# Kernel optimization log

Measured on AMD Instinct MI355X. Metric: run time of the kernel, lower is better.

The kernel has to match this reference:

```python
import jax, jax.numpy as jnp
import numpy as np

B, T, F, U, L, C = 1024, 100, 300, 512, 2, 10
EPS = 1e-3  # keras LayerNormalization default epsilon


def _ln(z, g, b):
    m = jnp.mean(z, axis=-1, keepdims=True)
    v = jnp.var(z, axis=-1, keepdims=True)
    return (z - m) * jax.lax.rsqrt(v + EPS) * g + b


def _cell(xt, h, c, W, R, bias, kg, kb, rg, rb, sg, sb):
    # LayerNormLSTMCell: LN(x@W) + LN(h@R) + b, gates i,f,g,o; LN on new cell state
    z = _ln(xt @ W, kg, kb) + _ln(h @ R, rg, rb) + bias
    i, f, g, o = jnp.split(z, 4, axis=-1)
    c_new = jax.nn.sigmoid(f) * c + jax.nn.sigmoid(i) * jnp.tanh(g)
    c_new = _ln(c_new, sg, sb)
    h_new = jax.nn.sigmoid(o) * jnp.tanh(c_new)
    return h_new, c_new


def setup_inputs() -> dict:
    key = jax.random.key(0)
    ks = jax.random.split(key, 8 + 2 * L)
    d = {}
    d["x"] = jax.random.normal(ks[0], (B, T, F), jnp.float32)
    lens = jax.random.randint(ks[1], (B,), 1, T + 1)
    d["mask"] = (jnp.arange(T)[None, :] < lens[:, None]).astype(jnp.int32)
    in_dims = [F, U]
    ki = 2
    for l in range(L):
        s = 1.0 / np.sqrt(in_dims[l])
        d[f"W{l}"] = jax.random.uniform(ks[ki], (in_dims[l], 4 * U), jnp.float32, -s, s); ki += 1
        d[f"R{l}"] = jax.random.uniform(ks[ki], (U, 4 * U), jnp.float32, -0.044, 0.044); ki += 1
        d[f"b{l}"] = jnp.zeros((4 * U,), jnp.float32)
        d[f"kg{l}"] = jnp.ones((4 * U,), jnp.float32)
        d[f"kb{l}"] = jnp.zeros((4 * U,), jnp.float32)
        d[f"rg{l}"] = jnp.ones((4 * U,), jnp.float32)
        d[f"rb{l}"] = jnp.zeros((4 * U,), jnp.float32)
        d[f"sg{l}"] = jnp.ones((U,), jnp.float32)
        d[f"sb{l}"] = jnp.zeros((U,), jnp.float32)
    s = 1.0 / np.sqrt(U)
    d["Wd"] = jax.random.uniform(ks[ki], (U, C), jnp.float32, -s, s)
    d["bd"] = jnp.zeros((C,), jnp.float32)
    return d


def _forward(x, mask,
             W0, R0, b0, kg0, kb0, rg0, rb0, sg0, sb0,
             W1, R1, b1, kg1, kb1, rg1, rb1, sg1, sb1,
             Wd, bd):
    params = [
        (W0, R0, b0, kg0, kb0, rg0, rb0, sg0, sb0),
        (W1, R1, b1, kg1, kb1, rg1, rb1, sg1, sb1),
    ]
    bsz = x.shape[0]
    dt = x.dtype

    def step(carry, inp_t):
        states, out_prev = carry
        xt, mt = inp_t  # xt: [B,F], mt: [B] bool
        mb = mt[:, None]
        inp = xt
        new_states = []
        for (h, c), p in zip(states, params):
            hn, cn = _cell(inp, h, c, *p)
            inp = hn
            # Keras RNN masking: carry previous state at masked steps
            new_states.append((jnp.where(mb, hn, h), jnp.where(mb, cn, c)))
        out = jnp.where(mb, inp, out_prev)
        return (tuple(new_states), out), None

    init_states = tuple((jnp.zeros((bsz, U), dt), jnp.zeros((bsz, U), dt)) for _ in range(L))
    carry0 = (init_states, jnp.zeros((bsz, U), dt))
    xs = (jnp.transpose(x, (1, 0, 2)), mask.T.astype(bool))  # time-major
    (_, out), _ = jax.lax.scan(step, carry0, xs)
    return jax.nn.softmax(out @ Wd + bd, axis=-1)


def reference(x, mask,
              W0, R0, b0, kg0, kb0, rg0, rb0, sg0, sb0,
              W1, R1, b1, kg1, kb1, rg1, rb1, sg1, sb1,
              Wd, bd):
    return _forward(x, mask,
                    W0, R0, b0, kg0, kb0, rg0, rb0, sg0, sb0,
                    W1, R1, b1, kg1, kb1, rg1, rb1, sg1, sb1,
                    Wd, bd)
```

## Files before the change

### kernel.cpp

```cpp
#include <hip/hip_runtime.h>

#define B_ 1024
#define T_ 100
#define F_ 300
#define FP_ 320
#define U_ 512
#define G4_ 2048
#define C_ 10
#define EPS_ 1e-3f

typedef _Float16 f16x8 __attribute__((ext_vector_type(8)));
typedef float f32x4 __attribute__((ext_vector_type(4)));

typedef __attribute__((address_space(1))) const void* gcptr_t;
typedef __attribute__((address_space(3))) void* lptr_t;

__device__ __forceinline__ void async_ld16(_Float16* lds, const _Float16* g) {
  __builtin_amdgcn_global_load_lds((gcptr_t)g, (lptr_t)lds, 16, 0, 0);
}

__global__ __launch_bounds__(1024) void prep_kernel(const int* __restrict__ mask,
                                                    int* __restrict__ perm,
                                                    int* __restrict__ nt) {
  __shared__ int cnt[T_ + 1];
  __shared__ int start[T_ + 1];
  int b = threadIdx.x;
  if (b <= T_) cnt[b] = 0;
  __syncthreads();
  const int* mrow = mask + (size_t)b * T_;
  int len = 0;
  for (int t = 0; t < T_; t++) len += mrow[t];
  atomicAdd(&cnt[len], 1);
  __syncthreads();
  if (b == 0) {
    int run = 0;
    for (int l = T_; l >= 0; l--) {
      start[l] = run;
      run += cnt[l];
    }
  }
  __syncthreads();
  if (b < T_) nt[b] = start[b];
  __syncthreads();
  int pos = atomicAdd(&start[len], 1);
  perm[pos] = b;
}


__global__ __launch_bounds__(256) void cast_x_kernel(const float* __restrict__ x,
                                                     const int* __restrict__ perm,
                                                     const int* __restrict__ nt,
                                                     _Float16* __restrict__ xhi,
                                                     _Float16* __restrict__ xlo) {
  size_t cidx = (size_t)blockIdx.x * 256 + threadIdx.x;
  int fc = (int)(cidx % (FP_ / 8));
  size_t bt = cidx / (FP_ / 8);
  int i = (int)(bt % B_);
  int t = (int)(bt / B_);
  int nr = (nt[t] + 127) & ~127;
  if (i >= nr) return;
  int b = perm[i];
  int f = fc * 8;
  const float* xr = x + ((size_t)b * T_ + t) * F_;
  float v[8];
  if (f + 8 <= F_) {
    float4 a = *(const float4*)(xr + f);
    float4 c = *(const float4*)(xr + f + 4);
    v[0] = a.x; v[1] = a.y; v[2] = a.z; v[3] = a.w;
    v[4] = c.x; v[5] = c.y; v[6] = c.z; v[7] = c.w;
  } else {
#pragma unroll
    for (int j = 0; j < 8; j++) v[j] = (f + j < F_) ? xr[f + j] : 0.f;
  }
  f16x8 hi, lo;
#pragma unroll
  for (int j = 0; j < 8; j++) {
    _Float16 h = (_Float16)v[j];
    hi[j] = h;
    lo[j] = (_Float16)(v[j] - (float)h);
  }
  *(f16x8*)(xhi + cidx * 8) = hi;
  *(f16x8*)(xlo + cidx * 8) = lo;
}

__global__ __launch_bounds__(256) void cast_w_kernel(const float* __restrict__ W,
                                                     _Float16* __restrict__ Whi,
                                                     _Float16* __restrict__ Wlo,
                                                     int K, int N, int Kp) {
  __shared__ float tile[32][33];
  int n0 = blockIdx.x * 32, k0 = blockIdx.y * 32;
  int tx = threadIdx.x & 31, ty = threadIdx.x >> 5;
#pragma unroll
  for (int r = 0; r < 32; r += 8) {
    int k = k0 + ty + r;
    tile[ty + r][tx] = (k < K) ? W[(size_t)k * N + n0 + tx] : 0.f;
  }
  __syncthreads();
#pragma unroll
  for (int r = 0; r < 32; r += 8) {
    int n = n0 + ty + r, kk = k0 + tx;
    if (kk < Kp) {
      float v = tile[tx][ty + r];
      _Float16 h = (_Float16)v;
      Whi[(size_t)n * Kp + kk] = h;
      Wlo[(size_t)n * Kp + kk] = (_Float16)(v - (float)h);
    }
  }
}

struct GemmOp {
  const _Float16* A;
  const _Float16* Bt;
  float* G;
  int lda;
  int K;
  size_t aLo;
  int step;
};
struct G4Pack {
  GemmOp op[4];
  const int* nt;
};

__global__ __launch_bounds__(256) void gemm_phase(G4Pack P) {
  GemmOp op = P.op[blockIdx.z];
  const int mBase = blockIdx.y * 128, nBase = blockIdx.x * 128;
  if (mBase >= P.nt[op.step]) return;
  const int K = op.K, lda = op.lda;
  const _Float16* A = op.A;
  const _Float16* Bt = op.Bt;

  __shared__ __align__(16) _Float16 as[128][64];
  __shared__ __align__(16) _Float16 bs[128][64];

  const int tid = threadIdx.x;
  const int w = tid >> 6;
  const int lane = tid & 63;
  const int wm = (w & 1) << 6;
  const int wn = (w >> 1) << 6;

  f32x4 acc[4][4];
#pragma unroll
  for (int mt = 0; mt < 4; mt++)
#pragma unroll
    for (int nt2 = 0; nt2 < 4; nt2++) acc[mt][nt2] = (f32x4){0.f, 0.f, 0.f, 0.f};

  const size_t bLo = (size_t)G4_ * K;
#pragma unroll 1
  for (int s = 0; s < 3; s++) {
    const _Float16* Ap = A + ((s == 1) ? op.aLo : 0);
    const _Float16* Bp = Bt + ((s == 2) ? bLo : 0);
#pragma unroll 1
    for (int k0 = 0; k0 < K; k0 += 64) {
#pragma unroll
      for (int j = 0; j < 4; j++) {
        int i = (w << 2) + j;
        int idx = (i << 6) + lane;
        int row = idx >> 3;
        int cl = ((idx & 7) ^ (row & 7)) << 3;
        async_ld16(&as[0][0] + (i << 9),
                   Ap + (size_t)(mBase + row) * lda + k0 + cl);
      }
#pragma unroll
      for (int j = 0; j < 4; j++) {
        int i = (w << 2) + j;
        int idx = (i << 6) + lane;
        int row = idx >> 3;
        int cl = ((idx & 7) ^ (row & 7)) << 3;
        async_ld16(&bs[0][0] + (i << 9),
                   Bp + (size_t)(nBase + row) * K + k0 + cl);
      }
      __syncthreads();
#pragma unroll
      for (int q = 0; q < 2; q++) {
        f16x8 af[4], bf[4];
#pragma unroll
        for (int mt = 0; mt < 4; mt++) {
          int row = wm + (mt << 4) + (lane & 15);
          int p = ((q << 2) + (lane >> 4)) ^ (row & 7);
          af[mt] = *(const f16x8*)&as[row][p << 3];
        }
#pragma unroll
        for (int nt2 = 0; nt2 < 4; nt2++) {
          int row = wn + (nt2 << 4) + (lane & 15);
          int p = ((q << 2) + (lane >> 4)) ^ (row & 7);
          bf[nt2] = *(const f16x8*)&bs[row][p << 3];
        }
#pragma unroll
        for (int mt = 0; mt < 4; mt++)
#pragma unroll
          for (int nt2 = 0; nt2 < 4; nt2++)
            acc[mt][nt2] = __builtin_amdgcn_mfma_f32_16x16x32_f16(af[mt], bf[nt2], acc[mt][nt2], 0, 0, 0);
      }
      __syncthreads();
    }
  }
  int q4 = lane >> 4, c = lane & 15;
  float* G = op.G;
#pragma unroll
  for (int mt = 0; mt < 4; mt++)
#pragma unroll
    for (int nt2 = 0; nt2 < 4; nt2++)
#pragma unroll
      for (int r = 0; r < 4; r++) {
        int row = mBase + wm + (mt << 4) + (q4 << 2) + r;
        int col = nBase + wn + (nt2 << 4) + c;
        G[(size_t)row * G4_ + col] = acc[mt][nt2][r];
      }
}


__device__ __forceinline__ void block_reduce(float* v, int n, float* sred, int tid) {
  int lane = tid & 63, w = tid >> 6;
  for (int off = 32; off > 0; off >>= 1)
    for (int i = 0; i < n; i++) v[i] += __shfl_down(v[i], off, 64);
  if (lane == 0)
    for (int i = 0; i < n; i++) sred[w * 4 + i] = v[i];
  __syncthreads();
  if (tid == 0)
    for (int i = 0; i < n; i++) sred[16 + i] = sred[i] + sred[4 + i] + sred[8 + i] + sred[12 + i];
  __syncthreads();
  for (int i = 0; i < n; i++) v[i] = sred[16 + i];
}

__device__ __forceinline__ float sigm(float x) { return 1.f / (1.f + expf(-x)); }

struct CellOp {
  const float* Gx;
  const float* Gh;
  const float* bias;
  const float* kg;
  const float* kb;
  const float* rg;
  const float* rb;
  const float* sg;
  const float* sb;
  float* cS;
  _Float16* hP;
  _Float16* hnP;
  float* outb;
  int step;
};
struct C2Pack {
  CellOp op[2];
  const int* nt;
};

__global__ __launch_bounds__(256) void cell_phase(C2Pack P) {
  CellOp cp = P.op[blockIdx.x >> 10];
  int b = blockIdx.x & (B_ - 1);
  if (b >= P.nt[cp.step]) return;
  int tid = threadIdx.x;
  __shared__ float sred[20];
  const float* gx = cp.Gx + (size_t)b * G4_;
  const float* gh = cp.Gh + (size_t)b * G4_;
  float vx[8], vh[8];
  float s[4] = {0.f, 0.f, 0.f, 0.f};
#pragma unroll
  for (int i = 0; i < 8; i++) {
    int col = tid + (i << 8);
    float a = gx[col], d = gh[col];
    vx[i] = a;
    vh[i] = d;
    s[0] += a;
    s[1] += a * a;
    s[2] += d;
    s[3] += d * d;
  }
  block_reduce(s, 4, sred, tid);
  const float inv = 1.f / 2048.f;
  float m1 = s[0] * inv, m2 = s[2] * inv;
  float rs1 = rsqrtf(fmaxf(s[1] * inv - m1 * m1, 0.f) + EPS_);
  float rs2 = rsqrtf(fmaxf(s[3] * inv - m2 * m2, 0.f) + EPS_);
  float z[8];
#pragma unroll
  for (int i = 0; i < 8; i++) {
    int col = tid + (i << 8);
    z[i] = (vx[i] - m1) * rs1 * cp.kg[col] + cp.kb[col] +
           (vh[i] - m2) * rs2 * cp.rg[col] + cp.rb[col] + cp.bias[col];
  }
  int j0 = tid, j1 = tid + 256;
  size_t base = (size_t)b * U_;
  _Float16* hHi = cp.hP;
  _Float16* hLo = cp.hP + (size_t)B_ * U_;
  float co0 = cp.cS[base + j0], co1 = cp.cS[base + j1];
  float cn0 = sigm(z[2]) * co0 + sigm(z[0]) * tanhf(z[4]);
  float cn1 = sigm(z[3]) * co1 + sigm(z[1]) * tanhf(z[5]);
  float t2[2] = {cn0 + cn1, cn0 * cn0 + cn1 * cn1};
  block_reduce(t2, 2, sred, tid);
  const float invU = 1.f / 512.f;
  float mc = t2[0] * invU;
  float rsc = rsqrtf(fmaxf(t2[1] * invU - mc * mc, 0.f) + EPS_);
  float cl0 = (cn0 - mc) * rsc * cp.sg[j0] + cp.sb[j0];
  float cl1 = (cn1 - mc) * rsc * cp.sg[j1] + cp.sb[j1];
  float hn0 = sigm(z[6]) * tanhf(cl0);
  float hn1 = sigm(z[7]) * tanhf(cl1);
  _Float16 hh0 = (_Float16)hn0, hh1 = (_Float16)hn1;
  hHi[base + j0] = hh0;
  hLo[base + j0] = (_Float16)(hn0 - (float)hh0);
  hHi[base + j1] = hh1;
  hLo[base + j1] = (_Float16)(hn1 - (float)hh1);
  cp.cS[base + j0] = cl0;
  cp.cS[base + j1] = cl1;
  if (cp.hnP) {
    _Float16* nHi = cp.hnP;
    _Float16* nLo = cp.hnP + (size_t)B_ * U_;
    nHi[base + j0] = hh0;
    nLo[base + j0] = (_Float16)(hn0 - (float)hh0);
    nHi[base + j1] = hh1;
    nLo[base + j1] = (_Float16)(hn1 - (float)hh1);
  }
  if (cp.outb) {
    cp.outb[base + j0] = hn0;
    cp.outb[base + j1] = hn1;
  }
}

__global__ __launch_bounds__(64) void dense_softmax_kernel(const float* __restrict__ outb,
                                                           const float* __restrict__ Wd,
                                                           const float* __restrict__ bd,
                                                           const int* __restrict__ perm,
                                                           float* __restrict__ o) {
  int b = blockIdx.x, lane = threadIdx.x;
  __shared__ float sl[16];
  int col = lane & 15, kg = lane >> 4;
  float acc = 0.f;
  if (col < C_) {
    for (int k = kg; k < U_; k += 4) acc += outb[(size_t)b * U_ + k] * Wd[(size_t)k * C_ + col];
  }
  acc += __shfl_down(acc, 16, 64);
  acc += __shfl_down(acc, 32, 64);
  if (lane < C_) sl[lane] = acc + bd[lane];
  __syncthreads();
  if (lane < C_) {
    float mx = sl[0];
    for (int i = 1; i < C_; i++) mx = fmaxf(mx, sl[i]);
    float ssum = 0.f;
    for (int i = 0; i < C_; i++) ssum += expf(sl[i] - mx);
    o[(size_t)perm[b] * C_ + lane] = expf(sl[lane] - mx) / ssum;
  }
}


extern "C" void kernel_launch(void* const* d_in, const int* in_sizes, int n_in,
                              void* d_out, int out_size, void* d_ws, size_t ws_size,
                              hipStream_t stream) {
  const float* x = (const float*)d_in[0];
  const int* mask = (const int*)d_in[1];
  const float* W0 = (const float*)d_in[2];
  const float* R0 = (const float*)d_in[3];
  const float* b0 = (const float*)d_in[4];
  const float* kg0 = (const float*)d_in[5];
  const float* kb0 = (const float*)d_in[6];
  const float* rg0 = (const float*)d_in[7];
  const float* rb0 = (const float*)d_in[8];
  const float* sg0 = (const float*)d_in[9];
  const float* sb0 = (const float*)d_in[10];
  const float* W1 = (const float*)d_in[11];
  const float* R1 = (const float*)d_in[12];
  const float* b1 = (const float*)d_in[13];
  const float* kg1 = (const float*)d_in[14];
  const float* kb1 = (const float*)d_in[15];
  const float* rg1 = (const float*)d_in[16];
  const float* rb1 = (const float*)d_in[17];
  const float* sg1 = (const float*)d_in[18];
  const float* sb1 = (const float*)d_in[19];
  const float* Wd = (const float*)d_in[20];
  const float* bd = (const float*)d_in[21];
  float* out = (float*)d_out;

  char* w = (char*)d_ws;
  size_t o = 0;
  auto alloc = [&](size_t bytes) {
    size_t r = o;
    o += (bytes + 255) & ~(size_t)255;
    return r;
  };
  size_t o_c0s = alloc((size_t)B_ * U_ * 4);
  size_t o_c1s = alloc((size_t)B_ * U_ * 4);
  size_t o_outf = alloc((size_t)B_ * U_ * 4);
  size_t o_h0p = alloc((size_t)B_ * U_ * 2 * 2);
  size_t o_h1p = alloc((size_t)B_ * U_ * 2 * 2);
  size_t o_G0h = alloc((size_t)B_ * G4_ * 4);
  size_t zero_bytes = o;
  size_t o_hn0p = alloc((size_t)B_ * U_ * 2 * 2);
  size_t o_xh = alloc((size_t)T_ * B_ * FP_ * 2 * 2);
  size_t o_W0t = alloc((size_t)G4_ * FP_ * 2 * 2);
  size_t o_R0t = alloc((size_t)G4_ * U_ * 2 * 2);
  size_t o_W1t = alloc((size_t)G4_ * U_ * 2 * 2);
  size_t o_R1t = alloc((size_t)G4_ * U_ * 2 * 2);
  size_t o_G0x = alloc((size_t)B_ * G4_ * 4);
  size_t o_G1x = alloc((size_t)B_ * G4_ * 4);
  size_t o_G1h = alloc((size_t)B_ * G4_ * 4);
  size_t o_perm = alloc((size_t)B_ * 4);
  size_t o_nt = alloc((size_t)T_ * 4);
  (void)ws_size;

  float* c0s = (float*)(w + o_c0s);
  float* c1s = (float*)(w + o_c1s);
  float* outf = (float*)(w + o_outf);
  _Float16* h0p = (_Float16*)(w + o_h0p);
  _Float16* h1p = (_Float16*)(w + o_h1p);
  float* G0h = (float*)(w + o_G0h);
  _Float16* hn0p = (_Float16*)(w + o_hn0p);
  _Float16* xh = (_Float16*)(w + o_xh);
  _Float16* W0t = (_Float16*)(w + o_W0t);
  _Float16* R0t = (_Float16*)(w + o_R0t);
  _Float16* W1t = (_Float16*)(w + o_W1t);
  _Float16* R1t = (_Float16*)(w + o_R1t);
  float* G0x = (float*)(w + o_G0x);
  float* G1x = (float*)(w + o_G1x);
  float* G1h = (float*)(w + o_G1h);
  int* perm = (int*)(w + o_perm);
  int* ntp = (int*)(w + o_nt);

  hipMemsetAsync(w, 0, zero_bytes, stream);

  prep_kernel<<<1, 1024, 0, stream>>>(mask, perm, ntp);

  {
    size_t chunks = (size_t)T_ * B_ * (FP_ / 8);
    cast_x_kernel<<<dim3((unsigned)(chunks / 256)), 256, 0, stream>>>(
        x, perm, ntp, xh, xh + (size_t)T_ * B_ * FP_);
  }
  cast_w_kernel<<<dim3(G4_ / 32, FP_ / 32), 256, 0, stream>>>(
      W0, W0t, W0t + (size_t)G4_ * FP_, F_, G4_, FP_);
  cast_w_kernel<<<dim3(G4_ / 32, U_ / 32), 256, 0, stream>>>(
      R0, R0t, R0t + (size_t)G4_ * U_, U_, G4_, U_);
  cast_w_kernel<<<dim3(G4_ / 32, U_ / 32), 256, 0, stream>>>(
      W1, W1t, W1t + (size_t)G4_ * U_, U_, G4_, U_);
  cast_w_kernel<<<dim3(G4_ / 32, U_ / 32), 256, 0, stream>>>(
      R1, R1t, R1t + (size_t)G4_ * U_, U_, G4_, U_);

  const size_t xLoOff = (size_t)T_ * B_ * FP_;
  const size_t hLoOff = (size_t)B_ * U_;

  auto xw_op = [&](int t) -> GemmOp {
    return GemmOp{xh + (size_t)t * B_ * FP_, W0t, G0x, FP_, FP_, xLoOff, t};
  };
  CellOp cell0op = {G0x, G0h, b0, kg0, kb0, rg0, rb0, sg0, sb0,
                    c0s, h0p, hn0p, nullptr, 0};
  CellOp cell1op = {G1x, G1h, b1, kg1, kb1, rg1, rb1, sg1, sb1,
                    c1s, h1p, nullptr, outf, 0};

  {
    G4Pack P;
    P.nt = ntp;
    P.op[0] = xw_op(0);
    P.op[1] = P.op[0];
    P.op[2] = P.op[0];
    P.op[3] = P.op[0];
    gemm_phase<<<dim3(G4_ / 128, B_ / 128, 1), 256, 0, stream>>>(P);
    C2Pack CP;
    CP.nt = ntp;
    cell0op.step = 0;
    CP.op[0] = cell0op;
    CP.op[1] = cell0op;
    cell_phase<<<B_, 256, 0, stream>>>(CP);
  }

  for (int t = 0; t < T_; t++) {
    bool more = (t < T_ - 1);
    G4Pack P;
    P.nt = ntp;
    P.op[0] = GemmOp{hn0p, W1t, G1x, U_, U_, hLoOff, t};
    P.op[1] = GemmOp{h1p, R1t, G1h, U_, U_, hLoOff, t};
    if (more) {
      P.op[2] = GemmOp{h0p, R0t, G0h, U_, U_, hLoOff, t + 1};
      P.op[3] = xw_op(t + 1);
    } else {
      P.op[2] = P.op[0];
      P.op[3] = P.op[0];
    }
    gemm_phase<<<dim3(G4_ / 128, B_ / 128, more ? 4 : 2), 256, 0, stream>>>(P);

    C2Pack CP;
    CP.nt = ntp;
    cell1op.step = t;
    CP.op[0] = cell1op;
    cell0op.step = t + 1;
    CP.op[1] = more ? cell0op : cell1op;
    cell_phase<<<more ? 2 * B_ : B_, 256, 0, stream>>>(CP);
  }

  dense_softmax_kernel<<<B_, 64, 0, stream>>>(outf, Wd, bd, perm, out);
}
```

Measured before the change: 4.194 ms.

## Fuse split-fp16 hi/lo GEMM passes into a single K loop

The three sequential passes over K (hi*hi, lo*hi, hi*lo) become one loop. Each iteration loads the hi and lo tiles of both A and B into four LDS buffers and issues three MFMAs per fragment pair. This removes two extra K sweeps of loop overhead, barriers and redundant reloads of the hi tiles. It also raises MFMA priority with s_setprio. The cost is double the LDS footprint, 64KB per block, and more fragment registers, which may lower occupancy.

```diff
diff --git a/kernel.cpp b/kernel.cpp
--- a/kernel.cpp
+++ b/kernel.cpp
@@ -127,11 +127,15 @@
   const int mBase = blockIdx.y * 128, nBase = blockIdx.x * 128;
   if (mBase >= P.nt[op.step]) return;
   const int K = op.K, lda = op.lda;
-  const _Float16* A = op.A;
-  const _Float16* Bt = op.Bt;
-
-  __shared__ __align__(16) _Float16 as[128][64];
-  __shared__ __align__(16) _Float16 bs[128][64];
+  const _Float16* Ah = op.A;
+  const _Float16* Al = op.A + op.aLo;
+  const _Float16* Bh = op.Bt;
+  const _Float16* Bl = op.Bt + (size_t)G4_ * K;
+
+  __shared__ __align__(16) _Float16 ash[128][64];
+  __shared__ __align__(16) _Float16 asl[128][64];
+  __shared__ __align__(16) _Float16 bsh[128][64];
+  __shared__ __align__(16) _Float16 bsl[128][64];
 
   const int tid = threadIdx.x;
   const int w = tid >> 6;
@@ -145,55 +149,51 @@
 #pragma unroll
     for (int nt2 = 0; nt2 < 4; nt2++) acc[mt][nt2] = (f32x4){0.f, 0.f, 0.f, 0.f};
 
-  const size_t bLo = (size_t)G4_ * K;
 #pragma unroll 1
-  for (int s = 0; s < 3; s++) {
-    const _Float16* Ap = A + ((s == 1) ? op.aLo : 0);
-    const _Float16* Bp = Bt + ((s == 2) ? bLo : 0);
-#pragma unroll 1
-    for (int k0 = 0; k0 < K; k0 += 64) {
-#pragma unroll
-      for (int j = 0; j < 4; j++) {
-        int i = (w << 2) + j;
-        int idx = (i << 6) + lane;
-        int row = idx >> 3;
-        int cl = ((idx & 7) ^ (row & 7)) << 3;
-        async_ld16(&as[0][0] + (i << 9),
-                   Ap + (size_t)(mBase + row) * lda + k0 + cl);
+  for (int k0 = 0; k0 < K; k0 += 64) {
+#pragma unroll
+    for (int j = 0; j < 4; j++) {
+      int i = (w << 2) + j;
+      int idx = (i << 6) + lane;
+      int row = idx >> 3;
+      int cl = ((idx & 7) ^ (row & 7)) << 3;
+      size_t aoff = (size_t)(mBase + row) * lda + k0 + cl;
+      size_t boff = (size_t)(nBase + row) * K + k0 + cl;
+      async_ld16(&ash[0][0] + (i << 9), Ah + aoff);
+      async_ld16(&asl[0][0] + (i << 9), Al + aoff);
+      async_ld16(&bsh[0][0] + (i << 9), Bh + boff);
+      async_ld16(&bsl[0][0] + (i << 9), Bl + boff);
+    }
+    __syncthreads();
+#pragma unroll
+    for (int q = 0; q < 2; q++) {
+      f16x8 afh[4], afl[4], bfh[4], bfl[4];
+#pragma unroll
+      for (int mt = 0; mt < 4; mt++) {
+        int row = wm + (mt << 4) + (lane & 15);
+        int p = ((q << 2) + (lane >> 4)) ^ (row & 7);
+        afh[mt] = *(const f16x8*)&ash[row][p << 3];
+        afl[mt] = *(const f16x8*)&asl[row][p << 3];
       }
 #pragma unroll
-      for (int j = 0; j < 4; j++) {
-        int i = (w << 2) + j;
-        int idx = (i << 6) + lane;
-        int row = idx >> 3;
-        int cl = ((idx & 7) ^ (row & 7)) << 3;
-        async_ld16(&bs[0][0] + (i << 9),
-                   Bp + (size_t)(nBase + row) * K + k0 + cl);
+      for (int nt2 = 0; nt2 < 4; nt2++) {
+        int row = wn + (nt2 << 4) + (lane & 15);
+        int p = ((q << 2) + (lane >> 4)) ^ (row & 7);
+        bfh[nt2] = *(const f16x8*)&bsh[row][p << 3];
+        bfl[nt2] = *(const f16x8*)&bsl[row][p << 3];
       }
-      __syncthreads();
-#pragma unroll
-      for (int q = 0; q < 2; q++) {
-        f16x8 af[4], bf[4];
-#pragma unroll
-        for (int mt = 0; mt < 4; mt++) {
-          int row = wm + (mt << 4) + (lane & 15);
-          int p = ((q << 2) + (lane >> 4)) ^ (row & 7);
-          af[mt] = *(const f16x8*)&as[row][p << 3];
+      __builtin_amdgcn_s_setprio(1);
+#pragma unroll
+      for (int mt = 0; mt < 4; mt++)
+#pragma unroll
+        for (int nt2 = 0; nt2 < 4; nt2++) {
+          acc[mt][nt2] = __builtin_amdgcn_mfma_f32_16x16x32_f16(afh[mt], bfh[nt2], acc[mt][nt2], 0, 0, 0);
+          acc[mt][nt2] = __builtin_amdgcn_mfma_f32_16x16x32_f16(afl[mt], bfh[nt2], acc[mt][nt2], 0, 0, 0);
+          acc[mt][nt2] = __builtin_amdgcn_mfma_f32_16x16x32_f16(afh[mt], bfl[nt2], acc[mt][nt2], 0, 0, 0);
         }
-#pragma unroll
-        for (int nt2 = 0; nt2 < 4; nt2++) {
-          int row = wn + (nt2 << 4) + (lane & 15);
-          int p = ((q << 2) + (lane >> 4)) ^ (row & 7);
-          bf[nt2] = *(const f16x8*)&bs[row][p << 3];
-        }
-#pragma unroll
-        for (int mt = 0; mt < 4; mt++)
-#pragma unroll
-          for (int nt2 = 0; nt2 < 4; nt2++)
-            acc[mt][nt2] = __builtin_amdgcn_mfma_f32_16x16x32_f16(af[mt], bf[nt2], acc[mt][nt2], 0, 0, 0);
-      }
-      __syncthreads();
+      __builtin_amdgcn_s_setprio(0);
     }
+    __syncthreads();
   }
   int q4 = lane >> 4, c = lane & 15;
   float* G = op.G;
```

New measurement: 3.612 ms. -13.9%, faster.
